# Kernel tuning notes

Hardware: AMD Instinct MI355X
Metric: run time of the kernel (lower is better)

Reference implementation:

```python
import jax, jax.numpy as jnp
import numpy as np

NEGPOS_RATIO = 3


def setup_inputs() -> dict:
    key = jax.random.key(0)
    k1, k2, k3 = jax.random.split(key, 3)
    B, P, NUM_ATTR, NUM_CLASSES = 64, 32768, 14, 10
    p = jax.random.normal(k1, (B, P, NUM_ATTR), dtype=jnp.float32)
    loc_t = jax.random.normal(k2, (B, P, 4), dtype=jnp.float32)
    conf_t = jax.random.randint(k3, (B, P), 0, NUM_CLASSES, dtype=jnp.int32)
    return {"p": p, "loc_t": loc_t, "conf_t": conf_t}


def reference(p, loc_t, conf_t):
    # p: [B, P, 4 + num_classes] concatenated loc + conf predictions
    loc_p = p[:, :, :4]
    conf_p = p[:, :, 4:]
    B, P = conf_t.shape

    pos = conf_t > 0                       # [B, P] positive anchor mask
    num_pos = jnp.sum(pos)                 # global scalar, as in original

    # Smooth-L1 (beta=1) summed over positive anchors
    diff = loc_p - loc_t
    ad = jnp.abs(diff)
    sl1 = jnp.where(ad < 1.0, 0.5 * diff * diff, ad - 0.5)
    loss_loc = jnp.sum(sl1 * pos[..., None].astype(sl1.dtype))

    # Per-anchor CE-style confidence loss: logsumexp - logit[target]
    lse = jax.nn.logsumexp(conf_p, axis=-1)                      # [B, P]
    tgt_logit = jnp.take_along_axis(conf_p, conf_t[..., None].astype(jnp.int32), axis=-1)[..., 0]
    ce_all = lse - tgt_logit                                     # [B, P]

    # Hard negative mining: zero positives, rank descending per image
    loss_c = jnp.where(pos, 0.0, ce_all)
    order = jnp.argsort(-loss_c, axis=1)   # descending sort indices
    rank = jnp.argsort(order, axis=1)      # rank of each anchor
    num_neg = jnp.clip(NEGPOS_RATIO * num_pos, None, P - num_pos)
    neg = rank < num_neg                   # [B, P]

    sel = pos | neg
    loss_c_sum = jnp.sum(ce_all * sel.astype(ce_all.dtype))

    return (loss_loc + loss_c_sum) / num_pos.astype(p.dtype)
```

## Files before the change

### kernel.cpp

```cpp
#include <hip/hip_runtime.h>

#define NB 64
#define NP 32768
#define NA 14
#define NC 10
#define NANCH (NB * NP)
#define TILE 256
#define TPB 8
#define MAIN_BLOCKS (NANCH / (TILE * TPB))

#define ACC_LOSS  (2 * MAIN_BLOCKS)
#define ACC_MINE  (2 * MAIN_BLOCKS + 1)
#define DONE_SLOT (2 * MAIN_BLOCKS + 2)

typedef const __attribute__((address_space(1))) void* gptr_t;
typedef __attribute__((address_space(3))) void* lptr_t;

__global__ __launch_bounds__(256) void ssd_main(
    const float* __restrict__ p,
    const float* __restrict__ loc_t,
    const int* __restrict__ conf_t,
    double* __restrict__ ws)
{
    __shared__ float sp[2][TILE * NA];

    const int tid  = threadIdx.x;
    const int lane = tid & 63, wid = tid >> 6;
    const size_t tile0 = (size_t)blockIdx.x * TPB;

    if (blockIdx.x == 0 && tid == 0) {
        ws[ACC_MINE] = 0.0;
        *reinterpret_cast<unsigned long long*>(ws + DONE_SLOT) = 0ull;
    }

    auto stage = [&](int b, size_t tidx) {
        const char* gsrc  = reinterpret_cast<const char*>(p + tidx * (TILE * NA));
        char*       sbase = reinterpret_cast<char*>(sp[b]);
#pragma unroll
        for (int k = 0; k < 3; ++k) {
            const int c0 = k * 256 + wid * 64;
            __builtin_amdgcn_global_load_lds(
                (gptr_t)(gsrc + (size_t)(c0 + lane) * 16),
                (lptr_t)(sbase + (size_t)c0 * 16), 16, 0, 0);
        }
        if (wid < 2) {
            const int c0 = 768 + wid * 64;
            __builtin_amdgcn_global_load_lds(
                (gptr_t)(gsrc + (size_t)(c0 + lane) * 16),
                (lptr_t)(sbase + (size_t)c0 * 16), 16, 0, 0);
        }
    };

    stage(0, tile0);
    float4 ltc = reinterpret_cast<const float4*>(loc_t)[tile0 * TILE + tid];
    int    tc  = conf_t[tile0 * TILE + tid];

    float lossAcc = 0.f;
    int   cntAcc  = 0;

#pragma unroll
    for (int it = 0; it < TPB; ++it) {
        __syncthreads();

        float4 ltn = ltc; int tn = tc;
        if (it + 1 < TPB) {
            stage((it + 1) & 1, tile0 + it + 1);
            const size_t nb = (tile0 + it + 1) * TILE;
            ltn = reinterpret_cast<const float4*>(loc_t)[nb + tid];
            tn  = conf_t[nb + tid];
        }

        const float2* row =
            reinterpret_cast<const float2*>(&sp[it & 1][tid * NA]);
        float x[14];
#pragma unroll
        for (int j = 0; j < 7; ++j) {
            float2 w = row[j];
            x[2 * j]     = w.x;
            x[2 * j + 1] = w.y;
        }

        float m = x[4];
#pragma unroll
        for (int j = 5; j < 14; ++j) m = fmaxf(m, x[j]);
        float s = 0.f;
#pragma unroll
        for (int j = 4; j < 14; ++j) s += __expf(x[j] - m);
        float lse = m + __logf(s);

        float tgt = x[4];
#pragma unroll
        for (int j = 1; j < 10; ++j) tgt = (tc == j) ? x[4 + j] : tgt;
        float ce = lse - tgt;

        if (tc > 0) {
            float l = ce;
            const float* ltf = reinterpret_cast<const float*>(&ltc);
#pragma unroll
            for (int j = 0; j < 4; ++j) {
                float d  = x[j] - ltf[j];
                float ad = fabsf(d);
                l += (ad < 1.f) ? (0.5f * d * d) : (ad - 0.5f);
            }
            lossAcc += l;
            ++cntAcc;
        }
        ltc = ltn; tc = tn;
    }

    double dl = (double)lossAcc;
    int cnt = cntAcc;
#pragma unroll
    for (int off = 32; off > 0; off >>= 1) {
        dl  += __shfl_down(dl, off, 64);
        cnt += __shfl_down(cnt, off, 64);
    }
    __shared__ double sL[4];
    __shared__ int    sC[4];
    if (lane == 0) { sL[wid] = dl; sC[wid] = cnt; }
    __syncthreads();
    if (tid == 0) {
        ws[blockIdx.x] = sL[0] + sL[1] + sL[2] + sL[3];
        ws[MAIN_BLOCKS + blockIdx.x] =
            (double)(sC[0] + sC[1] + sC[2] + sC[3]);
    }
}

__device__ __forceinline__ float neg_conf_loss(
    const float* __restrict__ prow, const int* __restrict__ crow, int i)
{
    int t = crow[i];
    if (t > 0) return 0.f;
    const float* v = prow + (size_t)i * NA + 4;
    float m = v[0];
#pragma unroll
    for (int j = 1; j < NC; ++j) m = fmaxf(m, v[j]);
    float s = 0.f;
#pragma unroll
    for (int j = 0; j < NC; ++j) s += __expf(v[j] - m);
    return (m + __logf(s)) - v[0];
}

__global__ __launch_bounds__(256) void ssd_finish(
    const float* __restrict__ p,
    const int* __restrict__ conf_t,
    double* __restrict__ ws,
    float* __restrict__ out)
{
    const int tid = threadIdx.x;
    const int lane = tid & 63, wid = tid >> 6;
    __shared__ double sR[4];
    __shared__ double s_np;

    double c = 0.0;
    for (int i = tid; i < MAIN_BLOCKS; i += 256)
        c += ws[MAIN_BLOCKS + i];
#pragma unroll
    for (int off = 32; off > 0; off >>= 1)
        c += __shfl_down(c, off, 64);
    if (lane == 0) sR[wid] = c;
    __syncthreads();
    if (tid == 0) s_np = sR[0] + sR[1] + sR[2] + sR[3];
    __syncthreads();
    const double np_d = s_np;

    long long np = (long long)np_d;
    long long nn = 3 * np;
    long long ub = (long long)NP - np;
    if (ub < nn) nn = ub;

    auto base_loss = [&]() -> double {
        double l = 0.0;
        for (int i = tid; i < MAIN_BLOCKS; i += 256)
            l += ws[i];
#pragma unroll
        for (int off = 32; off > 0; off >>= 1)
            l += __shfl_down(l, off, 64);
        __shared__ double fL[4];
        if (lane == 0) fL[wid] = l;
        __syncthreads();
        return fL[0] + fL[1] + fL[2] + fL[3];
    };

    if (nn <= 0) {
        if (blockIdx.x == 0) {
            double L = base_loss();
            if (tid == 0) out[0] = (float)(L / np_d);
        }
        return;
    }

    const float* prow = p + (size_t)blockIdx.x * NP * NA;
    const int*   crow = conf_t + (size_t)blockIdx.x * NP;

    __shared__ unsigned int hist[256];
    __shared__ unsigned int s_prefix;
    __shared__ long long    s_want;

    unsigned int prefix = 0;
    long long want = nn;

    for (int pass = 0; pass < 4; ++pass) {
        int shift = 24 - 8 * pass;
        hist[tid] = 0;
        __syncthreads();
        for (int i = tid; i < NP; i += 256) {
            unsigned int k = __float_as_uint(neg_conf_loss(prow, crow, i));
            bool match = (pass == 0) || ((k >> (shift + 8)) == prefix);
            if (match) atomicAdd(&hist[(k >> shift) & 255u], 1u);
        }
        __syncthreads();
        if (tid == 0) {
            unsigned long long cum = 0;
            int d = 255;
            for (; d > 0; --d) {
                unsigned long long h = hist[d];
                if (cum + h >= (unsigned long long)want) break;
                cum += h;
            }
            s_want   = want - (long long)cum;
            s_prefix = (prefix << 8) | (unsigned int)d;
        }
        __syncthreads();
        prefix = s_prefix;
        want   = s_want;
        __syncthreads();
    }

    float T = __uint_as_float(prefix);
    double sgt = 0.0;
    long long cgt = 0;
    for (int i = tid; i < NP; i += 256) {
        float lc = neg_conf_loss(prow, crow, i);
        if (__float_as_uint(lc) > prefix) { sgt += (double)lc; ++cgt; }
    }
#pragma unroll
    for (int off = 32; off > 0; off >>= 1) {
        sgt += __shfl_down(sgt, off, 64);
        cgt += __shfl_down(cgt, off, 64);
    }
    __shared__ double    rL[4];
    __shared__ long long rC[4];
    if (lane == 0) { rL[wid] = sgt; rC[wid] = cgt; }
    __syncthreads();
    if (tid == 0) {
        double stot = rL[0] + rL[1] + rL[2] + rL[3];
        long long ctot = rC[0] + rC[1] + rC[2] + rC[3];
        double rowsum = stot + (double)(nn - ctot) * (double)T;
        atomicAdd(&ws[ACC_MINE], rowsum);
    }

    if (blockIdx.x == 0) {
        double L = base_loss();
        if (tid == 0) ws[ACC_LOSS] = L;
    }

    __threadfence();
    __shared__ unsigned int s_ticket;
    if (tid == 0)
        s_ticket = atomicAdd(reinterpret_cast<unsigned int*>(ws + DONE_SLOT), 1u);
    __syncthreads();
    if (s_ticket == NB - 1 && tid == 0) {
        double base  = __hip_atomic_load(&ws[ACC_LOSS], __ATOMIC_RELAXED,
                                         __HIP_MEMORY_SCOPE_AGENT);
        double mined = __hip_atomic_load(&ws[ACC_MINE], __ATOMIC_RELAXED,
                                         __HIP_MEMORY_SCOPE_AGENT);
        out[0] = (float)((base + mined) / np_d);
    }
}

extern "C" void kernel_launch(void* const* d_in, const int* in_sizes, int n_in,
                              void* d_out, int out_size, void* d_ws, size_t ws_size,
                              hipStream_t stream)
{
    const float* p      = (const float*)d_in[0];
    const float* loc_t  = (const float*)d_in[1];
    const int*   conf_t = (const int*)d_in[2];
    float*  out = (float*)d_out;
    double* ws  = (double*)d_ws;

    ssd_main<<<MAIN_BLOCKS, 256, 0, stream>>>(p, loc_t, conf_t, ws);
    ssd_finish<<<NB, 256, 0, stream>>>(p, conf_t, ws, out);
}
```

Baseline: 33.57 us.

## Give each wave a private LDS tile pipeline, replacing block barriers with vmcnt waits

Restructures the main kernel so that each wave stages and consumes its own 64-anchor tiles in LDS, double-buffered per wave. This removes the per-iteration __syncthreads in favour of explicit s_waitcnt vmcnt counts. The aim is to stop waves stalling on each other and to let loads overlap compute more freely. Correctness depends on the hand-counted vmcnt(7) matching the number of outstanding loads and on the implicit wave-level LDS visibility. The tail of the tile is now loaded with 4-byte global_load_lds.

New measurement: 32.96 us. Within noise of the previous version (-1.8%).

```diff
diff --git a/kernel.cpp b/kernel.cpp
--- a/kernel.cpp
+++ b/kernel.cpp
@@ -5,9 +5,11 @@
 #define NA 14
 #define NC 10
 #define NANCH (NB * NP)
-#define TILE 256
-#define TPB 8
-#define MAIN_BLOCKS (NANCH / (TILE * TPB))
+#define WAVES 4
+#define WTILE 64
+#define TPW 8
+#define APB (WAVES * WTILE * TPW)
+#define MAIN_BLOCKS (NANCH / APB)
 
 #define ACC_LOSS  (2 * MAIN_BLOCKS)
 #define ACC_MINE  (2 * MAIN_BLOCKS + 1)
@@ -22,56 +24,60 @@
     const int* __restrict__ conf_t,
     double* __restrict__ ws)
 {
-    __shared__ float sp[2][TILE * NA];
+    __shared__ float sp[2][WAVES][WTILE * NA];
 
     const int tid  = threadIdx.x;
     const int lane = tid & 63, wid = tid >> 6;
-    const size_t tile0 = (size_t)blockIdx.x * TPB;
 
     if (blockIdx.x == 0 && tid == 0) {
         ws[ACC_MINE] = 0.0;
         *reinterpret_cast<unsigned long long*>(ws + DONE_SLOT) = 0ull;
     }
 
-    auto stage = [&](int b, size_t tidx) {
-        const char* gsrc  = reinterpret_cast<const char*>(p + tidx * (TILE * NA));
-        char*       sbase = reinterpret_cast<char*>(sp[b]);
-#pragma unroll
-        for (int k = 0; k < 3; ++k) {
-            const int c0 = k * 256 + wid * 64;
+    const size_t wbase = (size_t)blockIdx.x * APB + (size_t)wid * (WTILE * TPW);
+
+    auto stage = [&](int b, int t) {
+        const char* gsrc = reinterpret_cast<const char*>(
+            p + (wbase + (size_t)t * WTILE) * NA);
+        char* rb = reinterpret_cast<char*>(&sp[b][wid][0]);
+#pragma unroll
+        for (int k = 0; k < 3; ++k)
             __builtin_amdgcn_global_load_lds(
-                (gptr_t)(gsrc + (size_t)(c0 + lane) * 16),
-                (lptr_t)(sbase + (size_t)c0 * 16), 16, 0, 0);
-        }
-        if (wid < 2) {
-            const int c0 = 768 + wid * 64;
+                (gptr_t)(gsrc + (size_t)(k * 64 + lane) * 16),
+                (lptr_t)(rb + (size_t)k * 1024), 16, 0, 0);
+#pragma unroll
+        for (int k = 0; k < 2; ++k)
             __builtin_amdgcn_global_load_lds(
-                (gptr_t)(gsrc + (size_t)(c0 + lane) * 16),
-                (lptr_t)(sbase + (size_t)c0 * 16), 16, 0, 0);
-        }
+                (gptr_t)(gsrc + 3072 + (size_t)k * 256 + (size_t)lane * 4),
+                (lptr_t)(rb + 3072 + (size_t)k * 256), 4, 0, 0);
     };
 
-    stage(0, tile0);
-    float4 ltc = reinterpret_cast<const float4*>(loc_t)[tile0 * TILE + tid];
-    int    tc  = conf_t[tile0 * TILE + tid];
+    stage(0, 0);
+    float4 ltc = reinterpret_cast<const float4*>(loc_t)[wbase + lane];
+    int    tc  = conf_t[wbase + lane];
 
     float lossAcc = 0.f;
     int   cntAcc  = 0;
 
 #pragma unroll
-    for (int it = 0; it < TPB; ++it) {
-        __syncthreads();
-
+    for (int it = 0; it < TPW; ++it) {
         float4 ltn = ltc; int tn = tc;
-        if (it + 1 < TPB) {
-            stage((it + 1) & 1, tile0 + it + 1);
-            const size_t nb = (tile0 + it + 1) * TILE;
-            ltn = reinterpret_cast<const float4*>(loc_t)[nb + tid];
-            tn  = conf_t[nb + tid];
-        }
-
-        const float2* row =
-            reinterpret_cast<const float2*>(&sp[it & 1][tid * NA]);
+        if (it + 1 < TPW) {
+            stage((it + 1) & 1, it + 1);
+            const size_t na = wbase + (size_t)(it + 1) * WTILE + lane;
+            ltn = reinterpret_cast<const float4*>(loc_t)[na];
+            tn  = conf_t[na];
+            __builtin_amdgcn_sched_barrier(0);
+            asm volatile("s_waitcnt vmcnt(7)" ::: "memory");
+            __builtin_amdgcn_sched_barrier(0);
+        } else {
+            __builtin_amdgcn_sched_barrier(0);
+            asm volatile("s_waitcnt vmcnt(0)" ::: "memory");
+            __builtin_amdgcn_sched_barrier(0);
+        }
+
+        const float2* row = reinterpret_cast<const float2*>(
+            &sp[it & 1][wid][lane * NA]);
         float x[14];
 #pragma unroll
         for (int j = 0; j < 7; ++j) {
```
